# Performance work log

Hardware: AMD Instinct MI355X
Metric: run time of the kernel (lower is better)

## Reference

```python
import jax, jax.numpy as jnp
import numpy as np
from jax import lax

ROUTE_SCALE = 1.0
TOPK = 2


def conv2d(x, w, stride=1, pad=1):
    # x: [B, Cin, H, W], w: [Cout, Cin, kh, kw]
    return lax.conv_general_dilated(
        x, w, window_strides=(stride, stride),
        padding=[(pad, pad), (pad, pad)],
        dimension_numbers=("NCHW", "OIHW", "NCHW"))


def setup_inputs() -> dict:
    key = jax.random.key(0)
    ks = jax.random.split(key, 6)
    B, Cin, Cout, H, W, E = 8, 32, 32, 256, 256, 8
    x = jax.random.normal(ks[0], (B, Cin, H, W), dtype=jnp.float32)
    gate_w = jax.random.normal(ks[1], (E, Cin, 3, 3), dtype=jnp.float32) * 0.05
    gate_bias = jnp.zeros((E,), dtype=jnp.float32)  # load-balance bias buffer (zero in eval)
    expert_w = jax.random.normal(ks[2], (E, Cout, Cin, 3, 3), dtype=jnp.float32) * 0.05
    expert_b = jax.random.normal(ks[3], (E, Cout), dtype=jnp.float32) * 0.05
    shared_w = jax.random.normal(ks[4], (Cout, Cin, 3, 3), dtype=jnp.float32) * 0.05
    shared_b = jax.random.normal(ks[5], (Cout,), dtype=jnp.float32) * 0.05
    return {"x": x, "gate_w": gate_w, "gate_bias": gate_bias,
            "expert_w": expert_w, "expert_b": expert_b,
            "shared_w": shared_w, "shared_b": shared_b}


def reference(x, gate_w, gate_bias, expert_w, expert_b, shared_w, shared_b):
    B, Cin, H, W = x.shape
    E, Cout = expert_w.shape[0], expert_w.shape[1]
    # ---- Gate: sigmoid(conv) -> per-pixel top-k over expert channel dim ----
    scores = jax.nn.sigmoid(conv2d(x, gate_w))                 # [B, E, H, W]
    biased = scores + gate_bias[None, :, None, None]
    st = jnp.moveaxis(scores, 1, -1)                            # [B, H, W, E]
    bt = jnp.moveaxis(biased, 1, -1)
    _, idx = lax.top_k(bt, TOPK)                                # [B, H, W, K]
    w = jnp.take_along_axis(st, idx, axis=-1)                   # gather raw scores
    w = jax.nn.softmax(w, axis=-1) * ROUTE_SCALE                # [B, H, W, K]
    # dense per-expert routing weight: sum_k w_k * onehot(idx_k)
    onehot = jax.nn.one_hot(idx, E, dtype=x.dtype)              # [B, H, W, K, E]
    dense = jnp.einsum('bhwk,bhwke->bhwe', w, onehot)           # [B, H, W, E]
    dense = jnp.moveaxis(dense, -1, 1)                          # [B, E, H, W]
    # ---- All expert convs as one stacked conv, masked accumulate ----
    ew = expert_w.reshape(E * Cout, Cin, 3, 3)
    eo = conv2d(x, ew) + expert_b.reshape(-1)[None, :, None, None]
    eo = eo.reshape(B, E, Cout, H, W)
    out = jnp.einsum('bechw,behw->bchw', eo, dense)
    # ---- Shared expert ----
    out = out + conv2d(x, shared_w) + shared_b[None, :, None, None]
    return out
```

## Files before the change

kernel.cpp:

```cpp
#include <hip/hip_runtime.h>

typedef __attribute__((ext_vector_type(8)))  short bf16x8;
typedef __attribute__((ext_vector_type(16))) float f32x16;

#define XIM (32*256*256)

__device__ __forceinline__ short f2bf(float f){
    unsigned int u = __builtin_bit_cast(unsigned int, f);
    u += 0x7fffu + ((u >> 16) & 1u);
    return (short)(u >> 16);
}
__device__ __forceinline__ float bf2f(short s){
    unsigned int u = ((unsigned int)(unsigned short)s) << 16;
    return __builtin_bit_cast(float, u);
}
__device__ __forceinline__ void glds16(const short* g, short* l){
    __builtin_amdgcn_global_load_lds(
        (const __attribute__((address_space(1))) unsigned int*)g,
        (__attribute__((address_space(3))) unsigned int*)l,
        16, 0, 0);
}

__global__ __launch_bounds__(256) void prep_weights(const float* __restrict__ ew,
                                                    const float* __restrict__ sw,
                                                    const float* __restrict__ ebv,
                                                    const float* __restrict__ sbv,
                                                    short* __restrict__ wt2){
    int i = blockIdx.x * 256 + threadIdx.x;
    if(i < 73728){
        int c7  = i & 7;
        int col = (i >> 3) & 31;
        int cio = (i >> 8) & 3;
        int rest = i >> 10;
        int tap = rest % 9;
        int es  = rest / 9;
        int ci  = cio*8 + c7;
        float v = ew[((es*32 + col)*32 + ci)*9 + tap] + sw[(col*32 + ci)*9 + tap];
        wt2[i] = f2bf(v);
    } else {
        int j = i - 73728, c = j >> 4, k = j & 15;
        float v = (k < 8) ? (ebv[k*32 + c] + sbv[c]) : 0.f;
        wt2[i] = f2bf(v);
    }
}

__global__ __launch_bounds__(256) void gate_kernel(const float* __restrict__ x,
                                                   const float* __restrict__ gw,
                                                   const float* __restrict__ gb,
                                                   short* __restrict__ route){
    __shared__ float xs[2][16][272];
    int raw = blockIdx.x;
    int wg  = (raw & 7)*128 + (raw >> 3);
    int b   = wg >> 7;
    int y0  = (wg & 127) * 2;
    int t   = threadIdx.x;
    int wv  = t >> 6, lane = t & 63;
    const float* xim = x + (size_t)b * XIM;

    if(t < 64){
        int bufi = t >> 5, s2 = (t >> 1) & 15;
        if(t & 1) xs[bufi][s2][260] = 0.f; else xs[bufi][s2][3] = 0.f;
    }

    auto STAGE = [&](int cc, int bufi){
        #pragma unroll
        for(int sg=0; sg<4; ++sg){
            int seg = wv*4 + sg;
            int r4  = seg >> 2, cid = seg & 3;
            int ci  = cc*4 + cid;
            int yy  = y0 - 1 + r4;
            const float* xr = xim + ((size_t)ci*256 + yy)*256;
            float4 v = make_float4(0.f,0.f,0.f,0.f);
            if(yy >= 0 && yy < 256) v = *(const float4*)(xr + lane*4);
            *(float4*)(&xs[bufi][seg][4 + lane*4]) = v;
        }
    };

    float g[2][8];
    #pragma unroll
    for(int pr=0;pr<2;++pr)
        #pragma unroll
        for(int e=0;e<8;++e) g[pr][e] = 0.f;

    STAGE(0, 0);
    __syncthreads();
    for(int cc=0; cc<8; ++cc){
        if(cc < 7) STAGE(cc+1, (cc+1)&1);
        const int bufi = cc & 1;
        #pragma unroll
        for(int cid=0; cid<4; ++cid){
            float sv[4][3];
            #pragma unroll
            for(int r4=0;r4<4;++r4){
                sv[r4][0] = xs[bufi][r4*4+cid][t+3];
                sv[r4][1] = xs[bufi][r4*4+cid][t+4];
                sv[r4][2] = xs[bufi][r4*4+cid][t+5];
            }
            const float* gwp = gw + (cc*4 + cid)*9;
            #pragma unroll
            for(int e=0;e<8;++e){
                #pragma unroll
                for(int kh=0;kh<3;++kh){
                    #pragma unroll
                    for(int kw=0;kw<3;++kw){
                        float wval = gwp[e*288 + kh*3 + kw];
                        g[0][e] = fmaf(sv[kh][kw],   wval, g[0][e]);
                        g[1][e] = fmaf(sv[kh+1][kw], wval, g[1][e]);
                    }
                }
            }
        }
        __syncthreads();
    }

    #pragma unroll
    for(int pr=0; pr<2; ++pr){
        float v1b=-1e30f, v2b=-1e30f, v3b=-1e30f, r1=0.f, r2=0.f; int i1=-1, i2=-1;
        #pragma unroll
        for(int e=0;e<8;e++){
            float se = 1.f/(1.f + expf(-g[pr][e]));
            float be = se + gb[e];
            if(be > v1b){ v3b=v2b; v2b=v1b; r2=r1; i2=i1; v1b=be; r1=se; i1=e; }
            else if(be > v2b){ v3b=v2b; v2b=be; r2=se; i2=e; }
            else if(be > v3b){ v3b=be; }
        }
        if(v2b - v3b < 2e-5f){
            int y = y0 + pr;
            double gd[8];
            #pragma unroll
            for(int e=0;e<8;e++) gd[e] = 0.0;
            for(int ci=0; ci<32; ++ci){
                for(int kh=0; kh<3; ++kh){
                    int yy = y + kh - 1;
                    if(yy < 0 || yy >= 256) continue;
                    const float* xr = xim + ((size_t)ci*256 + yy)*256;
                    for(int kw=0; kw<3; ++kw){
                        int xx = t + kw - 1;
                        if(xx < 0 || xx >= 256) continue;
                        double xv = (double)xr[xx];
                        const float* gwp = gw + ci*9 + kh*3 + kw;
                        #pragma unroll
                        for(int e=0;e<8;e++) gd[e] += xv * (double)gwp[e*288];
                    }
                }
            }
            double b1=-1e30, b2=-1e30; double rr1=0.0, rr2=0.0; int j1=-1, j2=-1;
            #pragma unroll
            for(int e=0;e<8;e++){
                double sd = 1.0/(1.0 + exp(-gd[e]));
                double bd = sd + (double)gb[e];
                if(bd > b1){ b2=b1; rr2=rr1; j2=j1; b1=bd; rr1=sd; j1=e; }
                else if(bd > b2){ b2=bd; rr2=sd; j2=e; }
            }
            i1=j1; i2=j2; r1=(float)rr1; r2=(float)rr2;
        }
        float m  = fmaxf(r1, r2);
        float e1 = expf(r1-m), e2 = expf(r2-m);
        float inv = 1.f/(e1+e2);
        float w1 = e1*inv, w2 = e2*inv;
        bf16x8 ov;
        #pragma unroll
        for(int e=0;e<8;e++){
            float dv = (e==i1) ? w1 : ((e==i2) ? w2 : 0.f);
            ov[e] = f2bf(dv);
        }
        *(bf16x8*)(route + ((size_t)(b*256 + y0 + pr)*256 + t)*8) = ov;
    }
}

__global__ __launch_bounds__(512, 2) void moe_main(const float* __restrict__ x,
                                                   const short* __restrict__ wt2,
                                                   const short* __restrict__ route,
                                                   float* __restrict__ out){
    __shared__ __align__(16) short wlds[73728];
    __shared__ __align__(16) short xt[10*2*34*8];
    int raw = blockIdx.x;
    int wg  = (raw & 7)*32 + (raw >> 3);
    int b   = wg >> 5;
    int y0  = (wg & 31) * 8;
    int t   = threadIdx.x;
    int wv  = t >> 6, l = t & 63, col = l & 31, hi = l >> 5;

    #pragma unroll
    for(int j=0;j<18;++j){
        int c = wv + 8*j;
        glds16(wt2 + c*512 + l*8, wlds + c*512);
    }

    const float* xim = x + (size_t)b*XIM;
    float* ob = out + (size_t)b*XIM;
    int yy = y0 + wv;
    bf16x8 biasA = *(const bf16x8*)(wt2 + 73728 + col*16 + hi*8);

    for(int tile=0; tile<8; ++tile){
        int x0 = tile*32;
        bf16x8 rfrag = *(const bf16x8*)(route + ((size_t)(b*256 + yy)*256 + x0 + col)*8);
        bf16x8 Bf[3][2][3];
        #pragma unroll
        for(int hf=0; hf<2; ++hf){
            __syncthreads();
            #pragma unroll
            for(int i=0;i<2;++i){
                int u = t + i*512;
                if(u < 640){
                    int px = u & 31, rc = u >> 5;
                    int row = rc >> 1, cic = rc & 1;
                    int cib = hf*16 + cic*8;
                    int ry = y0 - 1 + row, xx = x0 - 1 + px;
                    bool ok = (ry>=0 && ry<256 && xx>=0 && xx<256);
                    bf16x8 pk;
                    #pragma unroll
                    for(int j2=0;j2<8;++j2){
                        float v = ok ? xim[((size_t)(cib+j2)*256 + ry)*256 + xx] : 0.f;
                        pk[j2] = f2bf(v);
                    }
                    *(bf16x8*)(&xt[((row*2 + cic)*34 + px)*8]) = pk;
                }
            }
            if(t < 40){
                int pxh = 32 + (t & 1), rc = t >> 1;
                int row = rc >> 1, cic = rc & 1;
                int cib = hf*16 + cic*8;
                int ry = y0 - 1 + row, xx = x0 - 1 + pxh;
                bool ok = (ry>=0 && ry<256 && xx>=0 && xx<256);
                bf16x8 pk;
                #pragma unroll
                for(int j2=0;j2<8;++j2){
                    float v = ok ? xim[((size_t)(cib+j2)*256 + ry)*256 + xx] : 0.f;
                    pk[j2] = f2bf(v);
                }
                *(bf16x8*)(&xt[((row*2 + cic)*34 + pxh)*8]) = pk;
            }
            __syncthreads();
            #pragma unroll
            for(int kh=0;kh<3;++kh)
                #pragma unroll
                for(int kw=0;kw<3;++kw)
                    Bf[kh][hf][kw] = *(const bf16x8*)(&xt[(((wv+kh)*2 + hi)*34 + col + kw)*8]);
        }

        f32x16 z = {};
        f32x16 oa = __builtin_amdgcn_mfma_f32_32x32x16_bf16(biasA, rfrag, z, 0,0,0);
        #pragma unroll
        for(int es=0; es<8; ++es){
            f32x16 acc = {};
            #pragma unroll
            for(int tap=0; tap<9; ++tap){
                const int kh = tap/3, kw = tap - kh*3;
                #pragma unroll
                for(int hf=0; hf<2; ++hf){
                    bf16x8 a = *(const bf16x8*)(&wlds[(((es*9 + tap)*4 + hf*2 + hi)*32 + col)*8]);
                    acc = __builtin_amdgcn_mfma_f32_32x32x16_bf16(a, Bf[kh][hf][kw], acc, 0,0,0);
                }
            }
            float d = bf2f(rfrag[es]);
            #pragma unroll
            for(int r=0;r<16;r++) oa[r] += d*acc[r];
        }

        #pragma unroll
        for(int r=0;r<16;r++){
            int c = hi*4 + (r&3) + 8*(r>>2);
            ob[((size_t)c*256 + yy)*256 + x0 + col] = oa[r];
        }
    }
}

extern "C" void kernel_launch(void* const* d_in, const int* in_sizes, int n_in,
                              void* d_out, int out_size, void* d_ws, size_t ws_size,
                              hipStream_t stream){
    (void)in_sizes; (void)n_in; (void)out_size; (void)ws_size;
    const float* x   = (const float*)d_in[0];
    const float* gw  = (const float*)d_in[1];
    const float* gb  = (const float*)d_in[2];
    const float* ew  = (const float*)d_in[3];
    const float* ebv = (const float*)d_in[4];
    const float* sw  = (const float*)d_in[5];
    const float* sbv = (const float*)d_in[6];
    float* out = (float*)d_out;

    short* route = (short*)d_ws;
    short* wt2   = route + (size_t)8*256*256*8;

    prep_weights<<<dim3(290),  dim3(256), 0, stream>>>(ew, sw, ebv, sbv, wt2);
    gate_kernel <<<dim3(1024), dim3(256), 0, stream>>>(x, gw, gb, route);
    moe_main    <<<dim3(256),  dim3(512), 0, stream>>>(x, wt2, route, out);
}
```

Before: 252.3 us.

## Stream expert weights through small LDS buffer and double workgroup count

Replaces the full-resident expert weight LDS copy with a two-expert buffer reloaded per expert pair, and retiles each workgroup to 4 rows by 64 columns with 512 workgroups. This cuts LDS use so more workgroups can be resident per CU and halves per-block work. It adds repeated global-to-LDS weight reloads and extra barriers inside the compute loop with no double buffering.

```diff
diff --git a/kernel.cpp b/kernel.cpp
--- a/kernel.cpp
+++ b/kernel.cpp
@@ -172,96 +172,94 @@
                                                    const short* __restrict__ wt2,
                                                    const short* __restrict__ route,
                                                    float* __restrict__ out){
-    __shared__ __align__(16) short wlds[73728];
-    __shared__ __align__(16) short xt[10*2*34*8];
+    __shared__ __align__(16) short wbuf[18432];
+    __shared__ __align__(16) short xt[6*4*66*8];
     int raw = blockIdx.x;
-    int wg  = (raw & 7)*32 + (raw >> 3);
-    int b   = wg >> 5;
-    int y0  = (wg & 31) * 8;
+    int wg  = (raw & 7)*64 + (raw >> 3);
+    int b   = wg >> 6;
+    int y0  = (wg & 63) * 4;
     int t   = threadIdx.x;
     int wv  = t >> 6, l = t & 63, col = l & 31, hi = l >> 5;
-
-    #pragma unroll
-    for(int j=0;j<18;++j){
-        int c = wv + 8*j;
-        glds16(wt2 + c*512 + l*8, wlds + c*512);
-    }
+    int rr  = wv >> 1, hp = wv & 1;
 
     const float* xim = x + (size_t)b*XIM;
     float* ob = out + (size_t)b*XIM;
-    int yy = y0 + wv;
+    int yy = y0 + rr;
     bf16x8 biasA = *(const bf16x8*)(wt2 + 73728 + col*16 + hi*8);
 
-    for(int tile=0; tile<8; ++tile){
-        int x0 = tile*32;
-        bf16x8 rfrag = *(const bf16x8*)(route + ((size_t)(b*256 + yy)*256 + x0 + col)*8);
-        bf16x8 Bf[3][2][3];
-        #pragma unroll
-        for(int hf=0; hf<2; ++hf){
-            __syncthreads();
-            #pragma unroll
-            for(int i=0;i<2;++i){
-                int u = t + i*512;
-                if(u < 640){
-                    int px = u & 31, rc = u >> 5;
-                    int row = rc >> 1, cic = rc & 1;
-                    int cib = hf*16 + cic*8;
-                    int ry = y0 - 1 + row, xx = x0 - 1 + px;
-                    bool ok = (ry>=0 && ry<256 && xx>=0 && xx<256);
-                    bf16x8 pk;
-                    #pragma unroll
-                    for(int j2=0;j2<8;++j2){
-                        float v = ok ? xim[((size_t)(cib+j2)*256 + ry)*256 + xx] : 0.f;
-                        pk[j2] = f2bf(v);
-                    }
-                    *(bf16x8*)(&xt[((row*2 + cic)*34 + px)*8]) = pk;
-                }
-            }
-            if(t < 40){
-                int pxh = 32 + (t & 1), rc = t >> 1;
-                int row = rc >> 1, cic = rc & 1;
-                int cib = hf*16 + cic*8;
-                int ry = y0 - 1 + row, xx = x0 - 1 + pxh;
+    for(int ti=0; ti<4; ++ti){
+        int x0 = ti*64;
+        __syncthreads();
+        #pragma unroll
+        for(int j=0;j<5;++j){
+            int c = wv + 8*j;
+            if(c < 36) glds16(wt2 + c*512 + l*8, wbuf + c*512);
+        }
+        #pragma unroll
+        for(int i=0;i<4;++i){
+            int u = t + i*512;
+            if(u < 1584){
+                int rc = u / 66, px = u - rc*66;
+                int row = rc >> 2, cio = rc & 3;
+                int ry = y0 - 1 + row, xx = x0 - 1 + px;
                 bool ok = (ry>=0 && ry<256 && xx>=0 && xx<256);
                 bf16x8 pk;
                 #pragma unroll
                 for(int j2=0;j2<8;++j2){
-                    float v = ok ? xim[((size_t)(cib+j2)*256 + ry)*256 + xx] : 0.f;
+                    float v = ok ? xim[((size_t)(cio*8+j2)*256 + ry)*256 + xx] : 0.f;
                     pk[j2] = f2bf(v);
                 }
-                *(bf16x8*)(&xt[((row*2 + cic)*34 + pxh)*8]) = pk;
-            }
-            __syncthreads();
-            #pragma unroll
-            for(int kh=0;kh<3;++kh)
+                *(bf16x8*)(&xt[u*8]) = pk;
+            }
+        }
+        __syncthreads();
+
+        bf16x8 Bf[3][2][3];
+        #pragma unroll
+        for(int kh=0;kh<3;++kh)
+            #pragma unroll
+            for(int h2=0;h2<2;++h2)
                 #pragma unroll
                 for(int kw=0;kw<3;++kw)
-                    Bf[kh][hf][kw] = *(const bf16x8*)(&xt[(((wv+kh)*2 + hi)*34 + col + kw)*8]);
-        }
-
+                    Bf[kh][h2][kw] = *(const bf16x8*)(&xt[((((rr+kh)*4 + h2*2 + hi)*66 + hp*32 + col + kw))*8]);
+        bf16x8 rfrag = *(const bf16x8*)(route + ((size_t)(b*256 + yy)*256 + x0 + hp*32 + col)*8);
         f32x16 z = {};
         f32x16 oa = __builtin_amdgcn_mfma_f32_32x32x16_bf16(biasA, rfrag, z, 0,0,0);
-        #pragma unroll
-        for(int es=0; es<8; ++es){
-            f32x16 acc = {};
-            #pragma unroll
-            for(int tap=0; tap<9; ++tap){
-                const int kh = tap/3, kw = tap - kh*3;
-                #pragma unroll
-                for(int hf=0; hf<2; ++hf){
-                    bf16x8 a = *(const bf16x8*)(&wlds[(((es*9 + tap)*4 + hf*2 + hi)*32 + col)*8]);
-                    acc = __builtin_amdgcn_mfma_f32_32x32x16_bf16(a, Bf[kh][hf][kw], acc, 0,0,0);
-                }
-            }
-            float d = bf2f(rfrag[es]);
-            #pragma unroll
-            for(int r=0;r<16;r++) oa[r] += d*acc[r];
+
+        #pragma unroll
+        for(int p=0; p<4; ++p){
+            #pragma unroll
+            for(int e2=0; e2<2; ++e2){
+                f32x16 acc = {};
+                #pragma unroll
+                for(int tap=0; tap<9; ++tap){
+                    const int kh = tap/3, kw = tap - kh*3;
+                    #pragma unroll
+                    for(int h2=0; h2<2; ++h2){
+                        bf16x8 a = *(const bf16x8*)(&wbuf[(((e2*9 + tap)*4 + h2*2 + hi)*32 + col)*8]);
+                        acc = __builtin_amdgcn_mfma_f32_32x32x16_bf16(a, Bf[kh][h2][kw], acc, 0,0,0);
+                    }
+                }
+                float d = bf2f(rfrag[p*2 + e2]);
+                #pragma unroll
+                for(int r=0;r<16;r++) oa[r] += d*acc[r];
+            }
+            if(p < 3){
+                __syncthreads();
+                const short* src = wt2 + (p+1)*18432;
+                #pragma unroll
+                for(int j=0;j<5;++j){
+                    int c = wv + 8*j;
+                    if(c < 36) glds16(src + c*512 + l*8, wbuf + c*512);
+                }
+                __syncthreads();
+            }
         }
 
         #pragma unroll
         for(int r=0;r<16;r++){
             int c = hi*4 + (r&3) + 8*(r>>2);
-            ob[((size_t)c*256 + yy)*256 + x0 + col] = oa[r];
+            ob[((size_t)c*256 + yy)*256 + x0 + hp*32 + col] = oa[r];
         }
     }
 }
@@ -284,5 +282,5 @@
 
     prep_weights<<<dim3(290),  dim3(256), 0, stream>>>(ew, sw, ebv, sbv, wt2);
     gate_kernel <<<dim3(1024), dim3(256), 0, stream>>>(x, gw, gb, route);
-    moe_main    <<<dim3(256),  dim3(512), 0, stream>>>(x, wt2, route, out);
-}
+    moe_main    <<<dim3(512),  dim3(512), 0, stream>>>(x, wt2, route, out);
+}
```

Result: faster. 245.1 us (-2.8%).
